# Kernel tuning notes

Hardware: AMD Instinct MI355X
Metric: run time of the kernel (lower is better)

Reference implementation:

```python
import jax, jax.numpy as jnp
import numpy as np

D = 1024

def setup_inputs() -> dict:
    key = jax.random.key(0)
    ks = jax.random.split(key, 7)
    s = 1.0 / np.sqrt(D)  # torch Linear default init scale (uniform bound)
    x = jax.random.normal(ks[0], (4, 2048, D), dtype=jnp.float32)
    Wq = jax.random.uniform(ks[1], (D, D), jnp.float32, -s, s)
    Wk = jax.random.uniform(ks[2], (D, D), jnp.float32, -s, s)
    Wv = jax.random.uniform(ks[3], (D, D), jnp.float32, -s, s)
    bq = jax.random.uniform(ks[4], (D,), jnp.float32, -s, s)
    bk = jax.random.uniform(ks[5], (D,), jnp.float32, -s, s)
    bv = jax.random.uniform(ks[6], (D,), jnp.float32, -s, s)
    return {"x": x, "Wq": Wq, "bq": bq, "Wk": Wk, "bk": bk, "Wv": Wv, "bv": bv}

def reference(x, Wq, bq, Wk, bk, Wv, bv):
    # Linear layers: y = x @ W^T + b (weights stored torch-style [out, in])
    Q = jnp.einsum('bsd,ed->bse', x, Wq) + bq
    K = jnp.einsum('bsd,ed->bse', x, Wk) + bk
    V = jnp.einsum('bsd,ed->bse', x, Wv) + bv
    scale = jnp.sqrt(jnp.asarray(Q.shape[-1], Q.dtype))
    scores = jnp.einsum('bqd,bkd->bqk', Q, K) / scale  # [B, S, S]
    probs = jax.nn.softmax(scores, axis=-1)
    return jnp.einsum('bqk,bkd->bqd', probs, V)
```

## Files before the change

kernel.cpp:

```cpp
#include <hip/hip_runtime.h>


typedef __bf16 bf16x8 __attribute__((ext_vector_type(8)));
typedef float f32x4 __attribute__((ext_vector_type(4)));
typedef unsigned short u16;

__device__ __forceinline__ u16 f2b(float f) {
  union { float f; unsigned u; } a; a.f = f;
  unsigned r = a.u + 0x7fffu + ((a.u >> 16) & 1u);
  return (u16)(r >> 16);
}

__global__ __launch_bounds__(256) void cast_x_kernel(const float* __restrict__ in,
                                                     u16* __restrict__ out, int n4) {
  int i = blockIdx.x * 256 + threadIdx.x;
  if (i < n4) {
    float4 v = reinterpret_cast<const float4*>(in)[i];
    reinterpret_cast<ushort4*>(out)[i] =
        make_ushort4(f2b(v.x), f2b(v.y), f2b(v.z), f2b(v.w));
  }
}

__global__ __launch_bounds__(256) void cast_w_kernel(const float* __restrict__ Wq,
                                                     const float* __restrict__ Wk,
                                                     const float* __restrict__ Wv,
                                                     u16* __restrict__ out) {
  const int b = blockIdx.x;
  const int w = b >> 10;
  const float* src = (w == 0) ? Wq : (w == 1) ? Wk : Wv;
  const int i = (b & 1023) * 256 + threadIdx.x;
  float4 v = reinterpret_cast<const float4*>(src)[i];
  reinterpret_cast<ushort4*>(out + (size_t)w * 1048576)[i] =
      make_ushort4(f2b(v.x), f2b(v.y), f2b(v.z), f2b(v.w));
}

template <int GEOM, int NT>
__device__ __forceinline__ void core8(const char* __restrict__ Ab,
                                      const char* __restrict__ Bb, int lda, int ldb,
                                      char* smem, f32x4* acc) {
  constexpr int LDSBUF = GEOM ? 49152 : 65536;
  constexpr int BOFF = GEOM ? 16384 : 32768;
  constexpr int AHALF = GEOM ? 8192 : 16384;
  const int tid = threadIdx.x;
  const int wave = tid >> 6, lane = tid & 63;
  const int wr = wave >> 2, wc = wave & 3;
  const int fr = lane & 15, fg = lane >> 4;
  const int rd = (fr * 64 + fg * 16) ^ (((fr >> 3) & 1) << 5);
  const int li = (lane * 16) ^ ((lane >> 5) << 5);
  const int sr = li >> 6, sc2 = li & 63;

  auto STAGE = [&](int kt, int p) {
    const int isB = p & 1, s = p >> 1;
    char* lds = smem + (kt & 1) * LDSBUF + (isB ? BOFF + s * 16384 : s * AHALF);
    const char* gb = isB ? Bb : Ab;
    const int ldx = isB ? ldb : lda;
    const int colOff = kt * 128 + s * 64 + sc2;
    __builtin_amdgcn_global_load_lds(
        (const __attribute__((address_space(1))) void*)(gb + (size_t)(wave * 16 + sr) * ldx + colOff),
        (__attribute__((address_space(3))) void*)(lds + wave * 1024), 16, 0, 0);
    if (isB || GEOM == 0)
      __builtin_amdgcn_global_load_lds(
          (const __attribute__((address_space(1))) void*)(gb + (size_t)((8 + wave) * 16 + sr) * ldx + colOff),
          (__attribute__((address_space(3))) void*)(lds + 8192 + wave * 1024), 16, 0, 0);
  };

#pragma unroll
  for (int p = 0; p < 4; ++p) STAGE(0, p);
  STAGE(1, 0);
  STAGE(1, 1);
  if constexpr (GEOM == 0) asm volatile("s_waitcnt vmcnt(8)" ::: "memory");
  else asm volatile("s_waitcnt vmcnt(6)" ::: "memory");
  __builtin_amdgcn_s_barrier();
  __builtin_amdgcn_sched_barrier(0);

  bf16x8 keep[4];
  for (int kt = 0; kt < NT; ++kt) {
    const char* bufA = smem + (kt & 1) * LDSBUF;
    const char* bufB = bufA + BOFF;
#pragma unroll
    for (int p = 0; p < 4; ++p) {
      const int s = p >> 1, j = p & 1;
      if constexpr (GEOM == 0) {
        bf16x8 afr[4];
        if (j == 0)
#pragma unroll
          for (int n = 0; n < 4; ++n)
            keep[n] = *reinterpret_cast<const bf16x8*>(bufB + s * 16384 + (wc * 4 + n) * 1024 + rd);
#pragma unroll
        for (int m = 0; m < 4; ++m)
          afr[m] = *reinterpret_cast<const bf16x8*>(bufA + s * 16384 + (wr * 8 + j * 4 + m) * 1024 + rd);
        if (p < 2) { if (kt + 1 < NT) STAGE(kt + 1, p + 2); }
        else       { if (kt + 2 < NT) STAGE(kt + 2, p - 2); }
        __builtin_amdgcn_s_barrier();
        __builtin_amdgcn_sched_barrier(0);
        __builtin_amdgcn_s_setprio(1);
#pragma unroll
        for (int m = 0; m < 4; ++m)
#pragma unroll
          for (int n = 0; n < 4; ++n)
            acc[(j * 4 + m) * 4 + n] = __builtin_amdgcn_mfma_f32_16x16x32_bf16(
                afr[m], keep[n], acc[(j * 4 + m) * 4 + n], 0, 0, 0);
        __builtin_amdgcn_s_setprio(0);
      } else {
        bf16x8 bfr[2];
        if (j == 0)
#pragma unroll
          for (int m = 0; m < 4; ++m)
            keep[m] = *reinterpret_cast<const bf16x8*>(bufA + s * AHALF + (wr * 4 + m) * 1024 + rd);
#pragma unroll
        for (int nn = 0; nn < 2; ++nn)
          bfr[nn] = *reinterpret_cast<const bf16x8*>(bufB + s * 16384 + (wc * 4 + j * 2 + nn) * 1024 + rd);
        if (p < 2) { if (kt + 1 < NT) STAGE(kt + 1, p + 2); }
        else       { if (kt + 2 < NT) STAGE(kt + 2, p - 2); }
        __builtin_amdgcn_s_barrier();
        __builtin_amdgcn_sched_barrier(0);
        __builtin_amdgcn_s_setprio(1);
#pragma unroll
        for (int m = 0; m < 4; ++m)
#pragma unroll
          for (int nn = 0; nn < 2; ++nn)
            acc[m * 4 + j * 2 + nn] = __builtin_amdgcn_mfma_f32_16x16x32_bf16(
                keep[m], bfr[nn], acc[m * 4 + j * 2 + nn], 0, 0, 0);
        __builtin_amdgcn_s_setprio(0);
      }
      if (p == 1) {
        if (kt < NT - 1) {
          if constexpr (GEOM == 0) asm volatile("s_waitcnt vmcnt(8)" ::: "memory");
          else asm volatile("s_waitcnt vmcnt(6)" ::: "memory");
        } else {
          asm volatile("s_waitcnt vmcnt(0)" ::: "memory");
        }
      } else if (p == 3) {
        if (kt < NT - 2) {
          if constexpr (GEOM == 0) asm volatile("s_waitcnt vmcnt(8)" ::: "memory");
          else asm volatile("s_waitcnt vmcnt(6)" ::: "memory");
        } else if (kt == NT - 2) {
          if constexpr (GEOM == 0) asm volatile("s_waitcnt vmcnt(4)" ::: "memory");
          else asm volatile("s_waitcnt vmcnt(3)" ::: "memory");
        }
      }
      __builtin_amdgcn_s_barrier();
      __builtin_amdgcn_sched_barrier(0);
    }
  }
}

__global__ __launch_bounds__(512, 2) void proj8_kernel(
    const u16* __restrict__ A, const u16* __restrict__ Bm,
    const float* __restrict__ bq, const float* __restrict__ bk,
    const float* __restrict__ bvv, u16* __restrict__ QK, u16* __restrict__ Vt) {
  extern __shared__ char smem[];
  const int tileM = blockIdx.x * 256, tileN = blockIdx.y * 256;
  f32x4 acc[32] = {};
  core8<0, 16>((const char*)A + (size_t)tileM * 2048,
               (const char*)Bm + (size_t)tileN * 2048, 2048, 2048, smem, acc);
  const int tid = threadIdx.x;
  const int wave = tid >> 6, lane = tid & 63;
  const int wr = wave >> 2, wc = wave & 3, fr = lane & 15, fg = lane >> 4;
  const int w = blockIdx.y >> 2;
  const float* bias = (w == 0) ? bq : (w == 1) ? bk : bvv;
  if (w < 2) {
    u16* O = QK + (size_t)w * 8388608;
#pragma unroll
    for (int mi = 0; mi < 8; ++mi) {
      const int r0 = tileM + wr * 128 + mi * 16 + fg * 4;
#pragma unroll
      for (int n = 0; n < 4; ++n) {
        const int cw = (tileN + wc * 64 + n * 16 + fr) & 1023;
        const float bi = bias[cw];
#pragma unroll
        for (int jj = 0; jj < 4; ++jj)
          O[(size_t)(r0 + jj) * 1024 + cw] = f2b(acc[mi * 4 + n][jj] + bi);
      }
    }
  } else {
#pragma unroll
    for (int mi = 0; mi < 8; ++mi) {
      const int r0 = tileM + wr * 128 + mi * 16 + fg * 4;
      const int b = r0 >> 11, s0 = r0 & 2047;
#pragma unroll
      for (int n = 0; n < 4; ++n) {
        const int cw = (tileN + wc * 64 + n * 16 + fr) & 1023;
        const float bi = bias[cw];
        ushort4 u = make_ushort4(f2b(acc[mi * 4 + n][0] + bi), f2b(acc[mi * 4 + n][1] + bi),
                                 f2b(acc[mi * 4 + n][2] + bi), f2b(acc[mi * 4 + n][3] + bi));
        *reinterpret_cast<ushort4*>(&Vt[(size_t)b * 2097152 + (size_t)cw * 2048 + s0]) = u;
      }
    }
  }
}

__global__ __launch_bounds__(512, 2) void sc8_kernel(const u16* __restrict__ Qb,
                                                     const u16* __restrict__ Kb,
                                                     u16* __restrict__ P,
                                                     float* __restrict__ rowpart) {
  extern __shared__ char smem[];
  const int z = blockIdx.z;
  const int tileM = blockIdx.x * 256, tileN = blockIdx.y * 256;
  f32x4 acc[32] = {};
  core8<0, 16>((const char*)Qb + (size_t)z * 4194304 + (size_t)tileM * 2048,
               (const char*)Kb + (size_t)z * 4194304 + (size_t)tileN * 2048, 2048, 2048,
               smem, acc);
  const int tid = threadIdx.x;
  const int wave = tid >> 6, lane = tid & 63;
  const int wr = wave >> 2, wc = wave & 3, fr = lane & 15, fg = lane >> 4;
  float* rs = (float*)smem;
  u16* Po = P + (size_t)z * 4194304 + (size_t)tileM * 2048 + tileN;
#pragma unroll
  for (int mi = 0; mi < 8; ++mi) {
#pragma unroll
    for (int jj = 0; jj < 4; ++jj) {
      const int rl = wr * 128 + mi * 16 + fg * 4 + jj;
      float part = 0.f;
#pragma unroll
      for (int n = 0; n < 4; ++n) {
        float e = __expf(acc[mi * 4 + n][jj] * 0.03125f);
        part += e;
        Po[(size_t)rl * 2048 + wc * 64 + n * 16 + fr] = f2b(e);
      }
      part += __shfl_xor(part, 1);
      part += __shfl_xor(part, 2);
      part += __shfl_xor(part, 4);
      part += __shfl_xor(part, 8);
      if (fr == 0) rs[wc * 256 + rl] = part;
    }
  }
  __syncthreads();
  if (tid < 256) {
    float s = rs[tid] + rs[256 + tid] + rs[512 + tid] + rs[768 + tid];
    rowpart[(size_t)blockIdx.y * 8192 + z * 2048 + tileM + tid] = s;
  }
}

__global__ __launch_bounds__(256) void rsum_kernel(const float* __restrict__ rowpart,
                                                   float* __restrict__ rowinv) {
  const int i = blockIdx.x * 256 + threadIdx.x;
  float s = 0.f;
#pragma unroll
  for (int t = 0; t < 8; ++t) s += rowpart[t * 8192 + i];
  rowinv[i] = 1.0f / s;
}

__global__ __launch_bounds__(512, 2) void pv8_kernel(const u16* __restrict__ P,
                                                     const u16* __restrict__ Vt,
                                                     const float* __restrict__ rowinv,
                                                     float* __restrict__ out) {
  extern __shared__ char smem[];
  const int z = blockIdx.z;
  const int tileM = blockIdx.x * 128, tileN = blockIdx.y * 256;
  f32x4 acc[16] = {};
  core8<1, 32>((const char*)P + (size_t)z * 8388608 + (size_t)tileM * 4096,
               (const char*)Vt + (size_t)z * 4194304 + (size_t)tileN * 4096, 4096, 4096,
               smem, acc);
  const int tid = threadIdx.x;
  const int wave = tid >> 6, lane = tid & 63;
  const int wr = wave >> 2, wc = wave & 3, fr = lane & 15, fg = lane >> 4;
  float* O = out + (size_t)z * 2097152;
  const float* ri = rowinv + z * 2048 + tileM;
#pragma unroll
  for (int mi = 0; mi < 4; ++mi) {
#pragma unroll
    for (int jj = 0; jj < 4; ++jj) {
      const int r = wr * 64 + mi * 16 + fg * 4 + jj;
      const float inv = ri[r];
#pragma unroll
      for (int n = 0; n < 4; ++n)
        O[(size_t)(tileM + r) * 1024 + tileN + wc * 64 + n * 16 + fr] =
            acc[mi * 4 + n][jj] * inv;
    }
  }
}

extern "C" void kernel_launch(void* const* d_in, const int* in_sizes, int n_in,
                              void* d_out, int out_size, void* d_ws, size_t ws_size,
                              hipStream_t stream) {
  if (ws_size < ((size_t)72 << 20)) return;
  const float* x = (const float*)d_in[0];
  const float* Wq = (const float*)d_in[1];
  const float* bq = (const float*)d_in[2];
  const float* Wk = (const float*)d_in[3];
  const float* bk = (const float*)d_in[4];
  const float* Wv = (const float*)d_in[5];
  const float* bv = (const float*)d_in[6];
  char* ws = (char*)d_ws;
  u16* xb = (u16*)(ws);
  u16* Pb = (u16*)(ws);
  u16* Qb = (u16*)(ws + ((size_t)16 << 20));
  u16* Kb = (u16*)(ws + ((size_t)32 << 20));
  u16* Vt = (u16*)(ws + ((size_t)48 << 20));
  u16* Wb = (u16*)(ws + ((size_t)64 << 20));
  float* rowpart = (float*)(ws + ((size_t)70 << 20));
  float* rowinv = (float*)(ws + ((size_t)70 << 20) + 262144);
  float* out = (float*)d_out;

  (void)hipFuncSetAttribute((const void*)proj8_kernel,
                            hipFuncAttributeMaxDynamicSharedMemorySize, 131072);
  (void)hipFuncSetAttribute((const void*)sc8_kernel,
                            hipFuncAttributeMaxDynamicSharedMemorySize, 131072);
  (void)hipFuncSetAttribute((const void*)pv8_kernel,
                            hipFuncAttributeMaxDynamicSharedMemorySize, 98304);

  cast_x_kernel<<<8192, 256, 0, stream>>>(x, xb, 2097152);
  cast_w_kernel<<<3072, 256, 0, stream>>>(Wq, Wk, Wv, Wb);

  proj8_kernel<<<dim3(32, 12), 512, 131072, stream>>>(xb, Wb, bq, bk, bv, Qb, Vt);

  sc8_kernel<<<dim3(8, 8, 4), 512, 131072, stream>>>(Qb, Kb, Pb, rowpart);
  rsum_kernel<<<32, 256, 0, stream>>>(rowpart, rowinv);
  pv8_kernel<<<dim3(16, 4, 4), 512, 98304, stream>>>(Pb, Vt, rowinv, out);
}
```

Measured before the change: 160.8 us.

## Merge cast kernels, fold row-sum into PV, shrink projection tile

Merges the x and weight bf16 cast kernels into one launch, and removes the separate row-sum kernel by having each PV block reduce its own row partials into shared memory before the GEMM. The projection GEMM switches from a 256x256 tile to a 128x256 tile (the smaller GEOM), doubling the grid from 384 to 768 blocks to improve CU occupancy on a 256-CU device. This trades launch overhead and tail imbalance for lower per-block reuse in the projection. The rinv write into shared memory has no explicit barrier of its own and relies on barriers inside the GEMM core.

```diff
diff --git a/kernel.cpp b/kernel.cpp
--- a/kernel.cpp
+++ b/kernel.cpp
@@ -11,27 +11,27 @@
   return (u16)(r >> 16);
 }
 
-__global__ __launch_bounds__(256) void cast_x_kernel(const float* __restrict__ in,
-                                                     u16* __restrict__ out, int n4) {
-  int i = blockIdx.x * 256 + threadIdx.x;
-  if (i < n4) {
-    float4 v = reinterpret_cast<const float4*>(in)[i];
-    reinterpret_cast<ushort4*>(out)[i] =
+__global__ __launch_bounds__(256) void cast_all_kernel(const float* __restrict__ x,
+                                                       const float* __restrict__ Wq,
+                                                       const float* __restrict__ Wk,
+                                                       const float* __restrict__ Wv,
+                                                       u16* __restrict__ xb,
+                                                       u16* __restrict__ Wb) {
+  int b = blockIdx.x;
+  if (b < 8192) {
+    const int i = b * 256 + threadIdx.x;
+    float4 v = reinterpret_cast<const float4*>(x)[i];
+    reinterpret_cast<ushort4*>(xb)[i] =
         make_ushort4(f2b(v.x), f2b(v.y), f2b(v.z), f2b(v.w));
-  }
-}
-
-__global__ __launch_bounds__(256) void cast_w_kernel(const float* __restrict__ Wq,
-                                                     const float* __restrict__ Wk,
-                                                     const float* __restrict__ Wv,
-                                                     u16* __restrict__ out) {
-  const int b = blockIdx.x;
-  const int w = b >> 10;
-  const float* src = (w == 0) ? Wq : (w == 1) ? Wk : Wv;
-  const int i = (b & 1023) * 256 + threadIdx.x;
-  float4 v = reinterpret_cast<const float4*>(src)[i];
-  reinterpret_cast<ushort4*>(out + (size_t)w * 1048576)[i] =
-      make_ushort4(f2b(v.x), f2b(v.y), f2b(v.z), f2b(v.w));
+  } else {
+    b -= 8192;
+    const int w = b >> 10;
+    const float* src = (w == 0) ? Wq : (w == 1) ? Wk : Wv;
+    const int i = (b & 1023) * 256 + threadIdx.x;
+    float4 v = reinterpret_cast<const float4*>(src)[i];
+    reinterpret_cast<ushort4*>(Wb + (size_t)w * 1048576)[i] =
+        make_ushort4(f2b(v.x), f2b(v.y), f2b(v.z), f2b(v.w));
+  }
 }
 
 template <int GEOM, int NT>
@@ -150,9 +150,9 @@
     const float* __restrict__ bq, const float* __restrict__ bk,
     const float* __restrict__ bvv, u16* __restrict__ QK, u16* __restrict__ Vt) {
   extern __shared__ char smem[];
-  const int tileM = blockIdx.x * 256, tileN = blockIdx.y * 256;
-  f32x4 acc[32] = {};
-  core8<0, 16>((const char*)A + (size_t)tileM * 2048,
+  const int tileM = blockIdx.x * 128, tileN = blockIdx.y * 256;
+  f32x4 acc[16] = {};
+  core8<1, 16>((const char*)A + (size_t)tileM * 2048,
                (const char*)Bm + (size_t)tileN * 2048, 2048, 2048, smem, acc);
   const int tid = threadIdx.x;
   const int wave = tid >> 6, lane = tid & 63;
@@ -162,8 +162,8 @@
   if (w < 2) {
     u16* O = QK + (size_t)w * 8388608;
 #pragma unroll
-    for (int mi = 0; mi < 8; ++mi) {
-      const int r0 = tileM + wr * 128 + mi * 16 + fg * 4;
+    for (int mi = 0; mi < 4; ++mi) {
+      const int r0 = tileM + wr * 64 + mi * 16 + fg * 4;
 #pragma unroll
       for (int n = 0; n < 4; ++n) {
         const int cw = (tileN + wc * 64 + n * 16 + fr) & 1023;
@@ -175,8 +175,8 @@
     }
   } else {
 #pragma unroll
-    for (int mi = 0; mi < 8; ++mi) {
-      const int r0 = tileM + wr * 128 + mi * 16 + fg * 4;
+    for (int mi = 0; mi < 4; ++mi) {
+      const int r0 = tileM + wr * 64 + mi * 16 + fg * 4;
       const int b = r0 >> 11, s0 = r0 & 2047;
 #pragma unroll
       for (int n = 0; n < 4; ++n) {
@@ -232,37 +232,34 @@
   }
 }
 
-__global__ __launch_bounds__(256) void rsum_kernel(const float* __restrict__ rowpart,
-                                                   float* __restrict__ rowinv) {
-  const int i = blockIdx.x * 256 + threadIdx.x;
-  float s = 0.f;
-#pragma unroll
-  for (int t = 0; t < 8; ++t) s += rowpart[t * 8192 + i];
-  rowinv[i] = 1.0f / s;
-}
-
 __global__ __launch_bounds__(512, 2) void pv8_kernel(const u16* __restrict__ P,
                                                      const u16* __restrict__ Vt,
-                                                     const float* __restrict__ rowinv,
+                                                     const float* __restrict__ rowpart,
                                                      float* __restrict__ out) {
   extern __shared__ char smem[];
   const int z = blockIdx.z;
   const int tileM = blockIdx.x * 128, tileN = blockIdx.y * 256;
+  float* rinv = (float*)(smem + 98304);
+  const int tid = threadIdx.x;
+  if (tid < 128) {
+    float s = 0.f;
+#pragma unroll
+    for (int t = 0; t < 8; ++t) s += rowpart[t * 8192 + z * 2048 + tileM + tid];
+    rinv[tid] = 1.0f / s;
+  }
   f32x4 acc[16] = {};
   core8<1, 32>((const char*)P + (size_t)z * 8388608 + (size_t)tileM * 4096,
                (const char*)Vt + (size_t)z * 4194304 + (size_t)tileN * 4096, 4096, 4096,
                smem, acc);
-  const int tid = threadIdx.x;
   const int wave = tid >> 6, lane = tid & 63;
   const int wr = wave >> 2, wc = wave & 3, fr = lane & 15, fg = lane >> 4;
   float* O = out + (size_t)z * 2097152;
-  const float* ri = rowinv + z * 2048 + tileM;
 #pragma unroll
   for (int mi = 0; mi < 4; ++mi) {
 #pragma unroll
     for (int jj = 0; jj < 4; ++jj) {
       const int r = wr * 64 + mi * 16 + fg * 4 + jj;
-      const float inv = ri[r];
+      const float inv = rinv[r];
 #pragma unroll
       for (int n = 0; n < 4; ++n)
         O[(size_t)(tileM + r) * 1024 + tileN + wc * 64 + n * 16 + fr] =
@@ -290,22 +287,19 @@
   u16* Vt = (u16*)(ws + ((size_t)48 << 20));
   u16* Wb = (u16*)(ws + ((size_t)64 << 20));
   float* rowpart = (float*)(ws + ((size_t)70 << 20));
-  float* rowinv = (float*)(ws + ((size_t)70 << 20) + 262144);
   float* out = (float*)d_out;
 
   (void)hipFuncSetAttribute((const void*)proj8_kernel,
-                            hipFuncAttributeMaxDynamicSharedMemorySize, 131072);
+                            hipFuncAttributeMaxDynamicSharedMemorySize, 98304);
   (void)hipFuncSetAttribute((const void*)sc8_kernel,
                             hipFuncAttributeMaxDynamicSharedMemorySize, 131072);
   (void)hipFuncSetAttribute((const void*)pv8_kernel,
-                            hipFuncAttributeMaxDynamicSharedMemorySize, 98304);
-
-  cast_x_kernel<<<8192, 256, 0, stream>>>(x, xb, 2097152);
-  cast_w_kernel<<<3072, 256, 0, stream>>>(Wq, Wk, Wv, Wb);
-
-  proj8_kernel<<<dim3(32, 12), 512, 131072, stream>>>(xb, Wb, bq, bk, bv, Qb, Vt);
+                            hipFuncAttributeMaxDynamicSharedMemorySize, 98816);
+
+  cast_all_kernel<<<11264, 256, 0, stream>>>(x, Wq, Wk, Wv, xb, Wb);
+
+  proj8_kernel<<<dim3(64, 12), 512, 98304, stream>>>(xb, Wb, bq, bk, bv, Qb, Vt);
 
   sc8_kernel<<<dim3(8, 8, 4), 512, 131072, stream>>>(Qb, Kb, Pb, rowpart);
-  rsum_kernel<<<32, 256, 0, stream>>>(rowpart, rowinv);
-  pv8_kernel<<<dim3(16, 4, 4), 512, 98304, stream>>>(Pb, Vt, rowinv, out);
-}
+  pv8_kernel<<<dim3(16, 4, 4), 512, 98816, stream>>>(Pb, Vt, rowpart, out);
+}
```

Measured after the change: 155.7 us. -3.2%, faster.
